# Performance work log

Hardware: AMD Instinct MI355X
Metric: run time of the kernel (lower is better)

The kernel has to match this reference:

```python
import jax, jax.numpy as jnp
import numpy as np

ROPE_BASE = 10000.0

def rope_tables(n, r):
    inv = 1.0 / (ROPE_BASE ** (jnp.arange(0, r, 2, dtype=jnp.float32) / r))  # [r/2]
    ang = jnp.arange(n, dtype=jnp.float32)[:, None] * inv[None, :]           # [n, r/2]
    cos = jnp.concatenate([jnp.cos(ang), jnp.cos(ang)], axis=-1)             # [n, r]
    sin = jnp.concatenate([jnp.sin(ang), jnp.sin(ang)], axis=-1)
    return cos, sin

def apply_rope(x, cos, sin):
    # x: [B, H, T, r]; cos/sin: [T, r]
    half = x.shape[-1] // 2
    x_rot = jnp.concatenate([-x[..., half:], x[..., :half]], axis=-1)
    return x * cos + x_rot * sin

def setup_inputs() -> dict:
    key = jax.random.key(0)
    ks = jax.random.split(key, 8)
    B, S, L = 2, 1024, 1024
    dim_q, h, k, d_c, d_cq, r = 2048, 16, 128, 512, 1536, 64
    w = 0.02  # weight scale to keep activations numerically tame
    return {
        'hidden_q': jax.random.normal(ks[0], (B, S, dim_q), jnp.float32),
        'kv_c':     jax.random.normal(ks[1], (B, L, d_c), jnp.float32),
        'Wq':       jax.random.normal(ks[2], (h * k, dim_q), jnp.float32) * w,
        'w_kc_q':   jax.random.normal(ks[3], (h, k, d_cq), jnp.float32) * w,
        'W_qr':     jax.random.normal(ks[4], (h, d_cq, r), jnp.float32) * (w / np.sqrt(r)),
        'W_kr':     jax.random.normal(ks[5], (h, d_c, r), jnp.float32) * w,
        'w_kc_kv':  jax.random.normal(ks[6], (h, k, d_c), jnp.float32) * w,
        'Wo':       jax.random.normal(ks[7], (dim_q, h * k), jnp.float32) * w,
    }

def reference(hidden_q, kv_c, Wq, w_kc_q, W_qr, W_kr, w_kc_kv, Wo):
    B, S, _ = hidden_q.shape
    L = kv_c.shape[1]
    h, k, _ = w_kc_q.shape
    r = W_qr.shape[-1]
    # q projection: [B,S,h,k]
    q_hk = (hidden_q @ Wq.T).reshape(B, S, h, k)
    # low-rank expand to q-compressed space then retrieval space
    q_big = jnp.einsum('bshk,hkq->bshq', q_hk, w_kc_q)          # [B,S,h,d_cq]
    q_r = jnp.einsum('bshq,hqr->bhsr', q_big, W_qr)             # [B,h,S,r]
    k_r = jnp.einsum('bld,hdr->bhlr', kv_c, W_kr)               # [B,h,L,r]
    cos_S, sin_S = rope_tables(S, r)
    cos_L, sin_L = rope_tables(L, r)
    q_r = apply_rope(q_r, cos_S, sin_S)
    k_r = apply_rope(k_r, cos_L, sin_L)
    # attention in retrieval space, values are compressed kv (shared across heads)
    scores = jnp.einsum('bhsr,bhlr->bhsl', q_r, k_r)            # scale baked into W_qr
    attn = jax.nn.softmax(scores, axis=-1)
    ctx_c = jnp.einsum('bhsl,bld->bhsd', attn, kv_c)            # [B,h,S,d_c]
    # decompress per head: w_kc_kv is [h,k,d_c]
    ctx_lat = jnp.einsum('bhsd,hkd->bshk', ctx_c, w_kc_kv).reshape(B, S, h * k)
    return ctx_lat @ Wo.T
```

## Files before the change

kernel.cpp:

```cpp
#include <hip/hip_runtime.h>
#include <math.h>
#include <stdint.h>


typedef __attribute__((ext_vector_type(8))) short short8;
typedef __attribute__((ext_vector_type(4))) float f32x4;

#define GLOAD16(gsrc, ldst)                                                            \
  __builtin_amdgcn_global_load_lds((const __attribute__((address_space(1))) void*)(gsrc), \
                                   (__attribute__((address_space(3))) void*)(ldst), 16, 0, 0)

__device__ inline uint16_t f2b(float x) {
  uint32_t u = __builtin_bit_cast(uint32_t, x);
  u += 0x7fff + ((u >> 16) & 1);
  return (uint16_t)(u >> 16);
}
__device__ inline float b2f(uint16_t b) {
  uint32_t u = ((uint32_t)b) << 16;
  return __builtin_bit_cast(float, u);
}
__device__ inline uint32_t cvtpk_bf16(float lo, float hi) {
  uint32_t d;
  asm("v_cvt_pk_bf16_f32 %0, %1, %2" : "=v"(d) : "v"(lo), "v"(hi));
  return d;
}

__global__ __launch_bounds__(256) void convert5_kernel(
    const float* __restrict__ s0, uint16_t* __restrict__ t0, const float* __restrict__ s1,
    uint16_t* __restrict__ t1, const float* __restrict__ s2, uint16_t* __restrict__ t2,
    const float* __restrict__ s3, uint16_t* __restrict__ t3, const float* __restrict__ s4,
    uint16_t* __restrict__ t4) {
  int bid = blockIdx.x;
  const float* s;
  uint16_t* t;
  int off;
  if (bid < 2048) { s = s0; t = t0; off = bid; }
  else if (bid < 2560) { s = s1; t = t1; off = bid - 2048; }
  else if (bid < 3072) { s = s2; t = t2; off = bid - 2560; }
  else if (bid < 5120) { s = s3; t = t3; off = bid - 3072; }
  else { s = s4; t = t4; off = bid - 5120; }
  int i = off * 256 + threadIdx.x;
  const float4* s4v = (const float4*)s;
  float4 a = s4v[i * 2], b = s4v[i * 2 + 1];
  union {
    uint16_t u[8];
    uint4 v;
  } o;
  o.u[0] = f2b(a.x); o.u[1] = f2b(a.y); o.u[2] = f2b(a.z); o.u[3] = f2b(a.w);
  o.u[4] = f2b(b.x); o.u[5] = f2b(b.y); o.u[6] = f2b(b.z); o.u[7] = f2b(b.w);
  ((uint4*)t)[i] = o.v;
}

__global__ __launch_bounds__(256) void transpose_conv_kernel(const float* __restrict__ src,
                                                             uint16_t* __restrict__ dst,
                                                             int R, int C, int sOff, int dOff) {
  __shared__ float t[32][33];
  src += (size_t)blockIdx.z * sOff;
  dst += (size_t)blockIdx.z * dOff;
  int r0 = blockIdx.x * 32, c0 = blockIdx.y * 32;
  int tr = threadIdx.x >> 5, tc = threadIdx.x & 31;
#pragma unroll
  for (int i = 0; i < 4; ++i) t[tr + i * 8][tc] = src[(size_t)(r0 + tr + i * 8) * C + c0 + tc];
  __syncthreads();
#pragma unroll
  for (int i = 0; i < 4; ++i)
    dst[(size_t)(c0 + tr + i * 8) * R + r0 + tc] = f2b(t[tc][tr + i * 8]);
}

__global__ __launch_bounds__(64) void rope_tables_kernel(float* __restrict__ cosK,
                                                         float* __restrict__ sinK,
                                                         float* __restrict__ cosQ,
                                                         float* __restrict__ sinQ) {
  const float LOG2E = 1.44269504088896341f;
  int s = blockIdx.x;
  int j = threadIdx.x;
  int i = j & 31;
  float inv = powf(10000.0f, -(float)(2 * i) / 64.0f);
  float ang = (float)s * inv;
  float c = cosf(ang), sn = sinf(ang);
  cosK[s * 64 + j] = c;
  sinK[s * 64 + j] = sn;
  cosQ[s * 64 + j] = c * LOG2E;
  sinQ[s * 64 + j] = sn * LOG2E;
}

template <int BM, int EPI, int SPLITK = 1>
__global__ __launch_bounds__(256) void gemm_mfma_kernel(const uint16_t* __restrict__ A,
                                                        const uint16_t* __restrict__ Bt,
                                                        void* __restrict__ Cv, int K, int lda,
                                                        int ldb, int ldc, int aZ, int bZ, int cZ,
                                                        const float* __restrict__ rc,
                                                        const float* __restrict__ rs) {
  constexpr int MT = BM / 32;
  __shared__ __align__(16) uint16_t As[2][BM * 64];
  __shared__ __align__(16) uint16_t Bs[2][128 * 64];
  int z = blockIdx.z;
  if (SPLITK > 1) {
    int zh = z / SPLITK, zk = z % SPLITK;
    A += (size_t)zh * aZ + (size_t)zk * K;
    Bt += (size_t)zh * bZ + (size_t)zk * K;
  } else {
    A += (size_t)z * aZ;
    Bt += (size_t)z * bZ;
  }
  int m0 = blockIdx.x * BM, n0 = blockIdx.y * 128;
  int tid = threadIdx.x;
  int wave = tid >> 6, lane = tid & 63;
  int wm = wave >> 1, wn = wave & 1;
  int rS = lane >> 3, sl = lane & 7;
  int lr = lane >> 4, lc = lane & 15;

  auto stage = [&](int k0, int buf) {
#pragma unroll
    for (int i = 0; i < MT; ++i) {
      int idx = wave * MT + i;
      int row = idx * 8 + rS;
      GLOAD16(A + (size_t)(m0 + row) * lda + k0 + ((sl ^ (row & 7)) << 3),
              (uint8_t*)As[buf] + idx * 1024);
    }
#pragma unroll
    for (int i = 0; i < 4; ++i) {
      int idx = wave * 4 + i;
      int row = idx * 8 + rS;
      GLOAD16(Bt + (size_t)(n0 + row) * ldb + k0 + ((sl ^ (row & 7)) << 3),
              (uint8_t*)Bs[buf] + idx * 1024);
    }
  };

  f32x4 acc[MT][4] = {};
  stage(0, 0);
  int cur = 0;
  for (int k0 = 0; k0 < K; k0 += 64) {
    __syncthreads();
    if (k0 + 64 < K) stage(k0 + 64, cur ^ 1);
    short8 af[MT][2], bf[4][2];
#pragma unroll
    for (int t = 0; t < MT; ++t)
#pragma unroll
      for (int ks = 0; ks < 2; ++ks) {
        int slot = ks * 4 + lr;
        int ra = wm * (BM / 2) + t * 16 + lc;
        af[t][ks] =
            *(const short8*)((const uint8_t*)As[cur] + ra * 128 + ((slot ^ (ra & 7)) << 4));
      }
#pragma unroll
    for (int t = 0; t < 4; ++t)
#pragma unroll
      for (int ks = 0; ks < 2; ++ks) {
        int slot = ks * 4 + lr;
        int rb = wn * 64 + t * 16 + lc;
        bf[t][ks] =
            *(const short8*)((const uint8_t*)Bs[cur] + rb * 128 + ((slot ^ (rb & 7)) << 4));
      }
    __builtin_amdgcn_s_setprio(1);
#pragma unroll
    for (int mt = 0; mt < MT; ++mt)
#pragma unroll
      for (int nt = 0; nt < 4; ++nt) {
        acc[mt][nt] =
            __builtin_amdgcn_mfma_f32_16x16x32_bf16(af[mt][0], bf[nt][0], acc[mt][nt], 0, 0, 0);
        acc[mt][nt] =
            __builtin_amdgcn_mfma_f32_16x16x32_bf16(af[mt][1], bf[nt][1], acc[mt][nt], 0, 0, 0);
      }
    __builtin_amdgcn_s_setprio(0);
    cur ^= 1;
  }
  if (EPI == 3) {
#pragma unroll
    for (int mt = 0; mt < MT; ++mt)
#pragma unroll
      for (int nt = 0; nt < 4; ++nt)
#pragma unroll
        for (int r = 0; r < 4; ++r) {
          int m = m0 + wm * (BM / 2) + mt * 16 + lr * 4 + r;
          int n = n0 + wn * 64 + nt * 16 + lc;
          int pos = m & 1023, j = n & 63;
          float x = acc[mt][nt][r];
          float prt = acc[mt][nt ^ 2][r];
          float rot = (nt & 2) ? prt : -prt;
          float v = fmaf(x, rc[pos * 64 + j], rot * rs[pos * 64 + j]);
          ((uint16_t*)Cv)[(size_t)m * ldc + n] = f2b(v);
        }
  } else {
#pragma unroll
    for (int mt = 0; mt < MT; ++mt)
#pragma unroll
      for (int nt = 0; nt < 4; ++nt)
#pragma unroll
        for (int r = 0; r < 4; ++r) {
          int m = m0 + wm * (BM / 2) + mt * 16 + lr * 4 + r;
          int n = n0 + wn * 64 + nt * 16 + lc;
          float v = acc[mt][nt][r];
          if (EPI == 0)
            ((float*)Cv)[(size_t)z * cZ + (size_t)m * ldc + n] = v;
          else if (EPI == 1)
            ((uint16_t*)Cv)[(size_t)z * cZ + (size_t)m * ldc + n] = f2b(v);
          else
            ((uint16_t*)Cv)[((size_t)((m >> 10) * 2048 + n)) * 1024 + (m & 1023)] = f2b(v);
        }
  }
}

__global__ __launch_bounds__(256) void reduce1_kernel(const float* __restrict__ tp,
                                                      uint16_t* __restrict__ tmpT) {
  int gid = blockIdx.x * 256 + threadIdx.x;
  int zh = gid >> 13, e = gid & 8191;
  const float* b = tp + (size_t)zh * 32768 + e;
  tmpT[gid] = f2b(b[0] + b[8192] + b[16384] + b[24576]);
}

__global__ __launch_bounds__(256) void flash3_kernel(const uint16_t* __restrict__ qrb,
                                                     const uint16_t* __restrict__ krb,
                                                     const uint16_t* __restrict__ VhT,
                                                     uint16_t* __restrict__ ctxlatb) {
  __shared__ __align__(16) uint16_t Ks[2][64 * 64];
  __shared__ __align__(16) uint16_t Vs[2][128 * 64];
  __shared__ __align__(16) uint8_t Ps[4][16 * 144];
  int bh = blockIdx.x;
  int b = bh >> 4, h = bh & 15;
  int s0 = blockIdx.y * 64;
  int tid = threadIdx.x, wave = tid >> 6, lane = tid & 63;
  int lr = lane >> 4, lc = lane & 15;
  int rS = lane >> 3, sl = lane & 7;

  const uint16_t* qrow = qrb + (size_t)(b * 1024 + s0 + wave * 16 + lc) * 1024 + h * 64;
  short8 qa[2];
  qa[0] = *(const short8*)(qrow + lr * 8);
  qa[1] = *(const short8*)(qrow + 32 + lr * 8);

  float m_run = -1e30f, l_run = 0.f;
  f32x4 o[8] = {};

  uint8_t* psW = Ps[wave] + lc * 144 + lr * 8;
  const uint8_t* psR = Ps[wave] + lc * 144 + lr * 16;

  const uint16_t* krbase = krb + (size_t)(b * 1024) * 1024 + h * 64;
  const uint16_t* vtbase = VhT + (size_t)(b * 2048 + h * 128) * 1024;

  auto stageKV = [&](int l0, int buf) {
#pragma unroll
    for (int i = 0; i < 2; ++i) {
      int idx = wave * 2 + i;
      int row = idx * 8 + rS;
      GLOAD16(krbase + (size_t)(l0 + row) * 1024 + ((sl ^ (row & 7)) << 3),
              (uint8_t*)Ks[buf] + idx * 1024);
    }
#pragma unroll
    for (int i = 0; i < 4; ++i) {
      int idx = wave * 4 + i;
      int row = idx * 8 + rS;
      GLOAD16(vtbase + (size_t)row * 1024 + l0 + ((sl ^ (row & 7)) << 3),
              (uint8_t*)Vs[buf] + idx * 1024);
    }
  };

  stageKV(0, 0);
  int cur = 0;
  for (int l0 = 0; l0 < 1024; l0 += 64) {
    __syncthreads();
    if (l0 + 64 < 1024) stageKV(l0 + 64, cur ^ 1);

    f32x4 sc[4];
    __builtin_amdgcn_s_setprio(1);
#pragma unroll
    for (int nt = 0; nt < 4; ++nt) {
      int rowk = nt * 16 + lc;
      short8 kb0 =
          *(const short8*)((const uint8_t*)Ks[cur] + rowk * 128 + ((lr ^ (rowk & 7)) << 4));
      short8 kb1 =
          *(const short8*)((const uint8_t*)Ks[cur] + rowk * 128 + (((4 + lr) ^ (rowk & 7)) << 4));
      f32x4 z = {};
      z = __builtin_amdgcn_mfma_f32_16x16x32_bf16(kb0, qa[0], z, 0, 0, 0);
      sc[nt] = __builtin_amdgcn_mfma_f32_16x16x32_bf16(kb1, qa[1], z, 0, 0, 0);
    }
    __builtin_amdgcn_s_setprio(0);

    float mx = fmaxf(fmaxf(fmaxf(sc[0][0], sc[0][1]), fmaxf(sc[0][2], sc[0][3])),
                     fmaxf(fmaxf(sc[1][0], sc[1][1]), fmaxf(sc[1][2], sc[1][3])));
    float mx2 = fmaxf(fmaxf(fmaxf(sc[2][0], sc[2][1]), fmaxf(sc[2][2], sc[2][3])),
                      fmaxf(fmaxf(sc[3][0], sc[3][1]), fmaxf(sc[3][2], sc[3][3])));
    mx = fmaxf(mx, mx2);
    mx = fmaxf(mx, __shfl_xor(mx, 16));
    mx = fmaxf(mx, __shfl_xor(mx, 32));

    bool grow = mx > m_run + 8.0f;
    bool upd = (__ballot(grow) != 0ULL);
    float scale;
    if (upd) {
      float mn = fmaxf(m_run, mx);
      scale = exp2f(m_run - mn);
      m_run = mn;
    }

    float ps = 0.f;
#pragma unroll
    for (int nt = 0; nt < 4; ++nt) {
#pragma unroll
      for (int rp = 0; rp < 2; ++rp) {
        float p0 = exp2f(sc[nt][rp * 2] - m_run);
        float p1 = exp2f(sc[nt][rp * 2 + 1] - m_run);
        ps += p0 + p1;
        *(uint32_t*)(psW + nt * 32 + rp * 4) = cvtpk_bf16(p0, p1);
      }
    }
    ps += __shfl_xor(ps, 16);
    ps += __shfl_xor(ps, 32);

    if (upd) {
      l_run = l_run * scale + ps;
      float s0 = __shfl(scale, lr * 4 + 0);
      float s1 = __shfl(scale, lr * 4 + 1);
      float s2 = __shfl(scale, lr * 4 + 2);
      float s3 = __shfl(scale, lr * 4 + 3);
#pragma unroll
      for (int nt = 0; nt < 8; ++nt) {
        o[nt][0] *= s0;
        o[nt][1] *= s1;
        o[nt][2] *= s2;
        o[nt][3] *= s3;
      }
    } else {
      l_run += ps;
    }

    short8 pa[2];
    pa[0] = *(const short8*)(psR);
    pa[1] = *(const short8*)(psR + 64);
    __builtin_amdgcn_s_setprio(1);
#pragma unroll
    for (int nt = 0; nt < 8; ++nt) {
      int rowv = nt * 16 + lc;
      short8 vb0 =
          *(const short8*)((const uint8_t*)Vs[cur] + rowv * 128 + ((lr ^ (rowv & 7)) << 4));
      short8 vb1 =
          *(const short8*)((const uint8_t*)Vs[cur] + rowv * 128 + (((4 + lr) ^ (rowv & 7)) << 4));
      o[nt] = __builtin_amdgcn_mfma_f32_16x16x32_bf16(pa[0], vb0, o[nt], 0, 0, 0);
      o[nt] = __builtin_amdgcn_mfma_f32_16x16x32_bf16(pa[1], vb1, o[nt], 0, 0, 0);
    }
    __builtin_amdgcn_s_setprio(0);
    cur ^= 1;
  }
  float li[4];
#pragma unroll
  for (int r = 0; r < 4; ++r) li[r] = 1.0f / __shfl(l_run, lr * 4 + r);
  uint16_t* orow = ctxlatb + (size_t)(b * 1024 + s0 + wave * 16) * 2048 + h * 128;
#pragma unroll
  for (int nt = 0; nt < 8; ++nt)
#pragma unroll
    for (int r = 0; r < 4; ++r)
      orow[(size_t)(lr * 4 + r) * 2048 + nt * 16 + lc] = f2b(o[nt][r] * li[r]);
}

extern "C" void kernel_launch(void* const* d_in, const int* in_sizes, int n_in,
                              void* d_out, int out_size, void* d_ws, size_t ws_size,
                              hipStream_t stream) {
  const float* hidden_q = (const float*)d_in[0];
  const float* kv_c = (const float*)d_in[1];
  const float* Wq = (const float*)d_in[2];
  const float* w_kc_q = (const float*)d_in[3];
  const float* W_qr = (const float*)d_in[4];
  const float* W_kr = (const float*)d_in[5];
  const float* w_kc_kv = (const float*)d_in[6];
  const float* Wo = (const float*)d_in[7];
  float* out = (float*)d_out;

  const size_t MB = 1024 * 1024;
  uint8_t* base = (uint8_t*)d_ws;
  uint16_t* Wob = (uint16_t*)(base + 0 * MB);
  uint16_t* qrb = (uint16_t*)(base + 8 * MB);
  uint16_t* krb = (uint16_t*)(base + 12 * MB);
  uint16_t* VhT = (uint16_t*)(base + 16 * MB);
  uint16_t* ctxlatb = (uint16_t*)(base + 24 * MB);
  float* cosK = (float*)(base + 32 * MB);
  float* sinK = (float*)(base + 32 * MB + 262144);
  float* cosQ = (float*)(base + 32 * MB + 524288);
  float* sinQ = (float*)(base + 32 * MB + 786432);
  uint16_t* hqb = (uint16_t*)(base + 33 * MB);
  uint16_t* kvb = (uint16_t*)(base + 41 * MB);
  uint16_t* wkvb = (uint16_t*)(base + 43 * MB);
  uint16_t* WqT = (uint16_t*)(base + 45 * MB);
  uint16_t* WqrT = (uint16_t*)(base + 53 * MB);
  uint16_t* wkcqb = (uint16_t*)(base + 56 * MB);
  float* tmp1 = (float*)(base + 62 * MB);
  uint16_t* tmpT = (uint16_t*)(base + 64 * MB);
  uint16_t* WkrT = (uint16_t*)(base + 64 * MB + 262144);

  convert5_kernel<<<dim3(6656), dim3(256), 0, stream>>>(hidden_q, hqb, kv_c, kvb, w_kc_kv, wkvb,
                                                        Wo, Wob, w_kc_q, wkcqb);
  rope_tables_kernel<<<dim3(1024), dim3(64), 0, stream>>>(cosK, sinK, cosQ, sinQ);
  transpose_conv_kernel<<<dim3(48, 2, 16), dim3(256), 0, stream>>>((const float*)W_qr, WqrT, 1536,
                                                                   64, 98304, 98304);
  transpose_conv_kernel<<<dim3(64, 64, 1), dim3(256), 0, stream>>>(Wq, WqT, 2048, 2048, 0, 0);
  transpose_conv_kernel<<<dim3(16, 2, 16), dim3(256), 0, stream>>>((const float*)W_kr, WkrT, 512,
                                                                   64, 32768, 32768);
  gemm_mfma_kernel<64, 0, 4><<<dim3(1, 1, 64), dim3(256), 0, stream>>>(
      WqrT, wkcqb, tmp1, 384, 1536, 1536, 128, 98304, 196608, 8192, nullptr, nullptr);
  reduce1_kernel<<<dim3(512), dim3(256), 0, stream>>>(tmp1, tmpT);
  uint16_t* WfoldT = wkcqb;
  gemm_mfma_kernel<64, 1><<<dim3(1, 16, 16), dim3(256), 0, stream>>>(
      tmpT, WqT, WfoldT, 128, 128, 2048, 2048, 8192, 128, 131072, nullptr, nullptr);
  gemm_mfma_kernel<64, 3><<<dim3(32, 8), dim3(256), 0, stream>>>(hqb, WfoldT, qrb, 2048, 2048,
                                                                 2048, 1024, 0, 0, 0, cosQ, sinQ);
  gemm_mfma_kernel<64, 3><<<dim3(32, 8), dim3(256), 0, stream>>>(kvb, WkrT, krb, 512, 512, 512,
                                                                 1024, 0, 0, 0, cosK, sinK);
  gemm_mfma_kernel<64, 2><<<dim3(32, 16), dim3(256), 0, stream>>>(kvb, wkvb, VhT, 512, 512, 512, 0,
                                                                  0, 0, 0, nullptr, nullptr);
  flash3_kernel<<<dim3(32, 16), dim3(256), 0, stream>>>(qrb, krb, VhT, ctxlatb);
  gemm_mfma_kernel<64, 0><<<dim3(32, 16), dim3(256), 0, stream>>>(ctxlatb, Wob, out, 2048, 2048,
                                                                  2048, 2048, 0, 0, 0, nullptr,
                                                                  nullptr);
}
```

Before: 153.1 us.

## Split flash attention key range across two wave groups and merge partial softmax

The attention kernel now runs 512 threads per block, where two groups of four waves each process half of the 1024-key range for the same 64 query rows. The partial max and sum values are combined through LDS at the end, and one group adds the other group's rescaled output. The double-buffered K/V prefetch is replaced by single-buffered staging with two barriers per tile. This doubles the parallelism per query tile and halves the serial loop length, at the cost of losing load/compute overlap and using a larger LDS footprint (66KB per block).

Measured after the change: 151.0 us. No clear change (-1.4%).

```diff
diff --git a/kernel.cpp b/kernel.cpp
--- a/kernel.cpp
+++ b/kernel.cpp
@@ -209,21 +209,24 @@
   tmpT[gid] = f2b(b[0] + b[8192] + b[16384] + b[24576]);
 }
 
-__global__ __launch_bounds__(256) void flash3_kernel(const uint16_t* __restrict__ qrb,
-                                                     const uint16_t* __restrict__ krb,
-                                                     const uint16_t* __restrict__ VhT,
-                                                     uint16_t* __restrict__ ctxlatb) {
-  __shared__ __align__(16) uint16_t Ks[2][64 * 64];
-  __shared__ __align__(16) uint16_t Vs[2][128 * 64];
-  __shared__ __align__(16) uint8_t Ps[4][16 * 144];
+__global__ __launch_bounds__(512, 4) void flash3_kernel(const uint16_t* __restrict__ qrb,
+                                                        const uint16_t* __restrict__ krb,
+                                                        const uint16_t* __restrict__ VhT,
+                                                        uint16_t* __restrict__ ctxlatb) {
+  __shared__ __align__(16) uint8_t lds[67584];
   int bh = blockIdx.x;
   int b = bh >> 4, h = bh & 15;
   int s0 = blockIdx.y * 64;
   int tid = threadIdx.x, wave = tid >> 6, lane = tid & 63;
+  int ig = wave >> 2, w = wave & 3;
   int lr = lane >> 4, lc = lane & 15;
   int rS = lane >> 3, sl = lane & 7;
 
-  const uint16_t* qrow = qrb + (size_t)(b * 1024 + s0 + wave * 16 + lc) * 1024 + h * 64;
+  uint8_t* Ks = lds + ig * 8192;
+  uint8_t* Vs = lds + 16384 + ig * 16384;
+  uint8_t* Ps = lds + 49152 + wave * 2304;
+
+  const uint16_t* qrow = qrb + (size_t)(b * 1024 + s0 + w * 16 + lc) * 1024 + h * 64;
   short8 qa[2];
   qa[0] = *(const short8*)(qrow + lr * 8);
   qa[1] = *(const short8*)(qrow + 32 + lr * 8);
@@ -231,44 +234,40 @@
   float m_run = -1e30f, l_run = 0.f;
   f32x4 o[8] = {};
 
-  uint8_t* psW = Ps[wave] + lc * 144 + lr * 8;
-  const uint8_t* psR = Ps[wave] + lc * 144 + lr * 16;
+  uint8_t* psW = Ps + lc * 144 + lr * 8;
+  const uint8_t* psR = Ps + lc * 144 + lr * 16;
 
   const uint16_t* krbase = krb + (size_t)(b * 1024) * 1024 + h * 64;
   const uint16_t* vtbase = VhT + (size_t)(b * 2048 + h * 128) * 1024;
 
-  auto stageKV = [&](int l0, int buf) {
+  auto stageKV = [&](int l0) {
 #pragma unroll
     for (int i = 0; i < 2; ++i) {
-      int idx = wave * 2 + i;
+      int idx = w * 2 + i;
       int row = idx * 8 + rS;
-      GLOAD16(krbase + (size_t)(l0 + row) * 1024 + ((sl ^ (row & 7)) << 3),
-              (uint8_t*)Ks[buf] + idx * 1024);
+      GLOAD16(krbase + (size_t)(l0 + row) * 1024 + ((sl ^ (row & 7)) << 3), Ks + idx * 1024);
     }
 #pragma unroll
     for (int i = 0; i < 4; ++i) {
-      int idx = wave * 4 + i;
+      int idx = w * 4 + i;
       int row = idx * 8 + rS;
-      GLOAD16(vtbase + (size_t)row * 1024 + l0 + ((sl ^ (row & 7)) << 3),
-              (uint8_t*)Vs[buf] + idx * 1024);
+      GLOAD16(vtbase + (size_t)row * 1024 + l0 + ((sl ^ (row & 7)) << 3), Vs + idx * 1024);
     }
   };
 
-  stageKV(0, 0);
-  int cur = 0;
-  for (int l0 = 0; l0 < 1024; l0 += 64) {
+  for (int t = 0; t < 8; ++t) {
+    int l0 = ig * 512 + t * 64;
     __syncthreads();
-    if (l0 + 64 < 1024) stageKV(l0 + 64, cur ^ 1);
+    stageKV(l0);
+    __syncthreads();
 
     f32x4 sc[4];
     __builtin_amdgcn_s_setprio(1);
 #pragma unroll
     for (int nt = 0; nt < 4; ++nt) {
       int rowk = nt * 16 + lc;
-      short8 kb0 =
-          *(const short8*)((const uint8_t*)Ks[cur] + rowk * 128 + ((lr ^ (rowk & 7)) << 4));
-      short8 kb1 =
-          *(const short8*)((const uint8_t*)Ks[cur] + rowk * 128 + (((4 + lr) ^ (rowk & 7)) << 4));
+      short8 kb0 = *(const short8*)(Ks + rowk * 128 + ((lr ^ (rowk & 7)) << 4));
+      short8 kb1 = *(const short8*)(Ks + rowk * 128 + (((4 + lr) ^ (rowk & 7)) << 4));
       f32x4 z = {};
       z = __builtin_amdgcn_mfma_f32_16x16x32_bf16(kb0, qa[0], z, 0, 0, 0);
       sc[nt] = __builtin_amdgcn_mfma_f32_16x16x32_bf16(kb1, qa[1], z, 0, 0, 0);
@@ -308,16 +307,16 @@
 
     if (upd) {
       l_run = l_run * scale + ps;
-      float s0 = __shfl(scale, lr * 4 + 0);
-      float s1 = __shfl(scale, lr * 4 + 1);
-      float s2 = __shfl(scale, lr * 4 + 2);
-      float s3 = __shfl(scale, lr * 4 + 3);
+      float sc0 = __shfl(scale, lr * 4 + 0);
+      float sc1 = __shfl(scale, lr * 4 + 1);
+      float sc2 = __shfl(scale, lr * 4 + 2);
+      float sc3 = __shfl(scale, lr * 4 + 3);
 #pragma unroll
       for (int nt = 0; nt < 8; ++nt) {
-        o[nt][0] *= s0;
-        o[nt][1] *= s1;
-        o[nt][2] *= s2;
-        o[nt][3] *= s3;
+        o[nt][0] *= sc0;
+        o[nt][1] *= sc1;
+        o[nt][2] *= sc2;
+        o[nt][3] *= sc3;
       }
     } else {
       l_run += ps;
@@ -330,25 +329,49 @@
 #pragma unroll
     for (int nt = 0; nt < 8; ++nt) {
       int rowv = nt * 16 + lc;
-      short8 vb0 =
-          *(const short8*)((const uint8_t*)Vs[cur] + rowv * 128 + ((lr ^ (rowv & 7)) << 4));
-      short8 vb1 =
-          *(const short8*)((const uint8_t*)Vs[cur] + rowv * 128 + (((4 + lr) ^ (rowv & 7)) << 4));
+      short8 vb0 = *(const short8*)(Vs + rowv * 128 + ((lr ^ (rowv & 7)) << 4));
+      short8 vb1 = *(const short8*)(Vs + rowv * 128 + (((4 + lr) ^ (rowv & 7)) << 4));
       o[nt] = __builtin_amdgcn_mfma_f32_16x16x32_bf16(pa[0], vb0, o[nt], 0, 0, 0);
       o[nt] = __builtin_amdgcn_mfma_f32_16x16x32_bf16(pa[1], vb1, o[nt], 0, 0, 0);
     }
     __builtin_amdgcn_s_setprio(0);
-    cur ^= 1;
-  }
-  float li[4];
-#pragma unroll
-  for (int r = 0; r < 4; ++r) li[r] = 1.0f / __shfl(l_run, lr * 4 + r);
-  uint16_t* orow = ctxlatb + (size_t)(b * 1024 + s0 + wave * 16) * 2048 + h * 128;
-#pragma unroll
-  for (int nt = 0; nt < 8; ++nt)
-#pragma unroll
-    for (int r = 0; r < 4; ++r)
-      orow[(size_t)(lr * 4 + r) * 2048 + nt * 16 + lc] = f2b(o[nt][r] * li[r]);
+  }
+
+  __syncthreads();
+  float2* mlx = (float2*)(lds + 49152);
+  if (lr == 0) mlx[(ig * 4 + w) * 16 + lc] = make_float2(m_run, l_run);
+  __syncthreads();
+  float2 e0 = mlx[(0 * 4 + w) * 16 + lc];
+  float2 e1 = mlx[(1 * 4 + w) * 16 + lc];
+  float M = fmaxf(e0.x, e1.x);
+  float a0 = exp2f(e0.x - M), a1 = exp2f(e1.x - M);
+  float dinv = 1.0f / (e0.y * a0 + e1.y * a1);
+  float myA = ig ? a1 : a0;
+  float ar[4], dr[4];
+#pragma unroll
+  for (int r = 0; r < 4; ++r) {
+    ar[r] = __shfl(myA, lr * 4 + r);
+    dr[r] = __shfl(dinv, lr * 4 + r);
+  }
+  float* O1 = (float*)lds;
+  int qb = w * 16 + lr * 4;
+  if (ig == 1) {
+#pragma unroll
+    for (int nt = 0; nt < 8; ++nt)
+#pragma unroll
+      for (int r = 0; r < 4; ++r) O1[(qb + r) * 130 + nt * 16 + lc] = o[nt][r] * ar[r];
+  }
+  __syncthreads();
+  if (ig == 0) {
+    uint16_t* orow = ctxlatb + (size_t)(b * 1024 + s0 + w * 16) * 2048 + h * 128;
+#pragma unroll
+    for (int nt = 0; nt < 8; ++nt)
+#pragma unroll
+      for (int r = 0; r < 4; ++r) {
+        float v = (o[nt][r] * ar[r] + O1[(qb + r) * 130 + nt * 16 + lc]) * dr[r];
+        orow[(size_t)(lr * 4 + r) * 2048 + nt * 16 + lc] = f2b(v);
+      }
+  }
 }
 
 extern "C" void kernel_launch(void* const* d_in, const int* in_sizes, int n_in,
@@ -405,7 +428,7 @@
                                                                  1024, 0, 0, 0, cosK, sinK);
   gemm_mfma_kernel<64, 2><<<dim3(32, 16), dim3(256), 0, stream>>>(kvb, wkvb, VhT, 512, 512, 512, 0,
                                                                   0, 0, 0, nullptr, nullptr);
-  flash3_kernel<<<dim3(32, 16), dim3(256), 0, stream>>>(qrb, krb, VhT, ctxlatb);
+  flash3_kernel<<<dim3(32, 16), dim3(512), 0, stream>>>(qrb, krb, VhT, ctxlatb);
   gemm_mfma_kernel<64, 0><<<dim3(32, 16), dim3(256), 0, stream>>>(ctxlatb, Wob, out, 2048, 2048,
                                                                   2048, 2048, 0, 0, 0, nullptr,
                                                                   nullptr);
```
